# Optimization experiments

Hardware: AMD Instinct MI355X
Metric: run time of the kernel (lower is better)

Reference implementation:

```python
import jax, jax.numpy as jnp
import numpy as np

B = 8          # batch
HID = 1024     # hidden_size
NH = 8         # query heads
KVH = 1        # kv heads (GQA)
HD = 256       # head_dim
NL = 18        # layers
MLP = 4096     # intermediate size
AH = 50        # action_horizon (suffix len)
AD = 32        # action_dim
P = 1037       # prefix_len
EPS = 1e-6
ROPE_BASE = 10000.0
SCALE = HD ** -0.5
NEG = -2.3819763e38


def _rms(x):
    return x * jax.lax.rsqrt(jnp.mean(x * x, axis=-1, keepdims=True) + EPS)


def _ada_norm(x, cond, W):
    # AdaRMS: cond -> (scale, shift, gate); normed*(1+scale)+shift, gate returned for gated residual
    scale, shift, gate = jnp.split(cond @ W, 3, axis=-1)
    return _rms(x) * (1.0 + scale[:, None, :]) + shift[:, None, :], gate[:, None, :]


def _rope(x, pos):
    # x: [B, heads, S, HD], pos: [B, S]; HF rotate-half convention
    inv = 1.0 / (ROPE_BASE ** (jnp.arange(0, HD, 2, dtype=jnp.float32) / HD))
    freqs = pos[:, :, None].astype(jnp.float32) * inv          # [B,S,HD/2]
    cos = jnp.tile(jnp.cos(freqs), (1, 1, 2))[:, None]          # [B,1,S,HD]
    sin = jnp.tile(jnp.sin(freqs), (1, 1, 2))[:, None]
    x1, x2 = jnp.split(x, 2, axis=-1)
    return x * cos + jnp.concatenate([-x2, x1], axis=-1) * sin


def setup_inputs() -> dict:
    key = jax.random.key(0)
    ks = jax.random.split(key, 24)
    s = 0.02
    return {
        'prefix_keys': jax.random.normal(ks[0], (B, NL, KVH, P, HD), jnp.float32),
        'prefix_values': jax.random.normal(ks[1], (B, NL, KVH, P, HD), jnp.float32),
        'prefix_pad_masks': jnp.ones((B, P), dtype=bool),
        'x_t': jax.random.normal(ks[2], (B, AH, AD), jnp.float32),
        'timestep': jax.random.uniform(ks[3], (B,), jnp.float32),
        'Wq': jax.random.normal(ks[4], (NL, HID, NH * HD), jnp.float32) * s,
        'Wk': jax.random.normal(ks[5], (NL, HID, KVH * HD), jnp.float32) * s,
        'Wv': jax.random.normal(ks[6], (NL, HID, KVH * HD), jnp.float32) * s,
        'Wo': jax.random.normal(ks[7], (NL, NH * HD, HID), jnp.float32) * s,
        'Wg': jax.random.normal(ks[8], (NL, HID, MLP), jnp.float32) * s,
        'Wu': jax.random.normal(ks[9], (NL, HID, MLP), jnp.float32) * s,
        'Wd': jax.random.normal(ks[10], (NL, MLP, HID), jnp.float32) * s,
        'A1': jax.random.normal(ks[11], (NL, HID, 3 * HID), jnp.float32) * s,
        'A2': jax.random.normal(ks[12], (NL, HID, 3 * HID), jnp.float32) * s,
        'Af': jax.random.normal(ks[13], (HID, 3 * HID), jnp.float32) * s,
        'W_act_in': jax.random.normal(ks[14], (AD, HID), jnp.float32) * s,
        'b_act_in': jnp.zeros((HID,), jnp.float32),
        'W_act_out': jax.random.normal(ks[15], (HID, AD), jnp.float32) * s,
        'b_act_out': jnp.zeros((AD,), jnp.float32),
        'W_t_in': jax.random.normal(ks[16], (HID, HID), jnp.float32) * s,
        'b_t_in': jnp.zeros((HID,), jnp.float32),
        'W_t_out': jax.random.normal(ks[17], (HID, HID), jnp.float32) * s,
        'b_t_out': jnp.zeros((HID,), jnp.float32),
    }


def reference(prefix_keys, prefix_values, prefix_pad_masks, x_t, timestep,
              Wq, Wk, Wv, Wo, Wg, Wu, Wd, A1, A2, Af,
              W_act_in, b_act_in, W_act_out, b_act_out,
              W_t_in, b_t_in, W_t_out, b_t_out):
    b = x_t.shape[0]
    # --- time embedding (sinusoidal over log-spaced periods) -> AdaRMS cond ---
    frac = jnp.linspace(0.0, 1.0, HID // 2)
    period = 0.004 * (4.0 / 0.004) ** frac
    sin_in = (2.0 * jnp.pi / period)[None, :] * timestep[:, None]
    temb = jnp.concatenate([jnp.sin(sin_in), jnp.cos(sin_in)], axis=1)  # [B,HID]
    cond = jax.nn.silu(jax.nn.silu(temb @ W_t_in + b_t_in) @ W_t_out + b_t_out)

    # --- action input projection ---
    h = x_t @ W_act_in + b_act_in  # [B,AH,HID]

    # --- attention mask & positions ---
    # suffix att_masks = [1,0,...,0] -> cumsum constant -> suffix block fully visible
    suf_att = jnp.ones((b, AH, AH), dtype=bool)
    s2p = jnp.broadcast_to(prefix_pad_masks[:, None, :], (b, AH, P))
    full = jnp.concatenate([s2p, suf_att], axis=2)          # [B,AH,P+AH]
    bias = jnp.where(full, 0.0, NEG).astype(jnp.float32)[:, None]  # [B,1,AH,P+AH]
    offs = jnp.sum(prefix_pad_masks.astype(jnp.int32), axis=-1, keepdims=True)
    pos = offs + jnp.arange(AH)                              # [B,AH]

    def layer(hcur, p):
        wq, wk, wv, wo, wg, wu, wd, a1, a2, ck, cv = p
        normed, gate = _ada_norm(hcur, cond, a1)
        q = (normed @ wq).reshape(b, AH, NH, HD).transpose(0, 2, 1, 3)
        k = (normed @ wk).reshape(b, AH, KVH, HD).transpose(0, 2, 1, 3)
        v = (normed @ wv).reshape(b, AH, KVH, HD).transpose(0, 2, 1, 3)
        q = _rope(q, pos)
        k = _rope(k, pos)
        fk = jnp.concatenate([ck, k], axis=2)   # [B,KVH,P+AH,HD]
        fv = jnp.concatenate([cv, v], axis=2)
        rep = NH // KVH
        fk = jnp.repeat(fk, rep, axis=1)
        fv = jnp.repeat(fv, rep, axis=1)
        scores = jnp.einsum('bhqd,bhkd->bhqk', q, fk) * SCALE + bias
        attn = jax.nn.softmax(scores, axis=-1)
        o = jnp.einsum('bhqk,bhkd->bhqd', attn, fv)
        o = o.transpose(0, 2, 1, 3).reshape(b, AH, NH * HD) @ wo
        h1 = hcur + gate * o                     # gated residual 1
        n2, gate2 = _ada_norm(h1, cond, a2)
        mlp = (jax.nn.gelu(n2 @ wg, approximate=True) * (n2 @ wu)) @ wd
        return h1 + gate2 * mlp, None            # gated residual 2

    pk = jnp.moveaxis(prefix_keys, 1, 0)   # [NL,B,KVH,P,HD]
    pv = jnp.moveaxis(prefix_values, 1, 0)
    h, _ = jax.lax.scan(layer, h, (Wq, Wk, Wv, Wo, Wg, Wu, Wd, A1, A2, pk, pv))

    out, _ = _ada_norm(h, cond, Af)
    return out @ W_act_out + b_act_out  # [B,AH,AD]
```

## Files before the change

kernel.cpp:

```cpp
#include <hip/hip_runtime.h>

typedef unsigned short u16;
typedef unsigned int   u32;
typedef __attribute__((ext_vector_type(8))) short bh8;
typedef __attribute__((ext_vector_type(4))) float f4;

constexpr int BATCH = 8, HIDN = 1024, NHEAD = 8, HD = 256, NLAY = 18, DMLP = 4096;
constexpr int AHOR = 50, ADIMN = 32, PFXN = 1037, SEQN = 1087, NSTR = 17, MR = 400, MP = 512;
constexpr float EPSV = 1e-6f, NEGV = -2.3819763e38f, QSCALE = 0.0625f;
constexpr size_t ADASL = (size_t)37 * 3 * BATCH * HIDN;

static __device__ __forceinline__ u16 f2bf(float x){
  union{float f; u32 u;} v; v.f = x;
  u32 r = (v.u + 0x7FFFu + ((v.u >> 16) & 1u)) >> 16;
  return (u16)r;
}
static __device__ __forceinline__ float bf2f(u16 u){
  union{u32 u; float f;} v; v.u = ((u32)u) << 16; return v.f;
}
static __device__ __forceinline__ u32 pack2(float a, float b){
  return (u32)f2bf(a) | ((u32)f2bf(b) << 16);
}
static __device__ __forceinline__ f4 MFMA(bh8 a, bh8 b, f4 c){
  return __builtin_amdgcn_mfma_f32_16x16x32_bf16(a, b, c, 0, 0, 0);
}
static __device__ __forceinline__ float siluf_(float x){ return x / (1.f + __expf(-x)); }
static __device__ __forceinline__ float geluf_(float x){
  float y = 0.7978845608028654f * (x + 0.044715f * x * x * x);
  float e = __expf(2.f * y);
  return 0.5f * x * (2.f - 2.f / (e + 1.f));
}

__global__ void k_prep(const int* __restrict__ mask, const float* __restrict__ ts,
                       float* __restrict__ temb, int* __restrict__ offs,
                       float* __restrict__ ropec, float* __restrict__ ropes)
{
  int t = threadIdx.x;
  {
    int b = t >> 5, l = t & 31;
    const int* mp = mask + b * PFXN;
    int s = 0;
    for (int k = l; k < PFXN; k += 32) s += (mp[k] != 0);
    #pragma unroll
    for (int off = 16; off >= 1; off >>= 1) s += __shfl_xor(s, off);
    if (l == 0) offs[b] = s;
  }
  for (int i = t; i < BATCH * 512; i += 256){
    int b = i >> 9, j = i & 511;
    float frac = (float)j * (1.0f / 511.0f);
    float period = 0.004f * __expf(frac * 6.907755278982137f);
    float arg = (6.283185307179586f / period) * ts[b];
    float s, c; sincosf(arg, &s, &c);
    temb[b * HIDN + j] = s;
    temb[b * HIDN + 512 + j] = c;
  }
  __syncthreads();
  for (int i = t; i < BATCH * AHOR * 128; i += 256){
    int d = i & 127, bt = i >> 7, b = bt / AHOR, tt = bt % AHOR;
    float inv = __expf(-((float)d * (1.f / 128.f)) * 9.210340371976184f);
    float arg = (float)(offs[b] + tt) * inv;
    float s, c; sincosf(arg, &s, &c);
    ropec[i] = c; ropes[i] = s;
  }
}

__global__ void k_tproj(const float* __restrict__ X, const float* __restrict__ W,
                        const float* __restrict__ bias, float* __restrict__ out)
{
  __shared__ float xs[BATCH * HIDN];
  __shared__ float red[BATCH][8][32];
  int t = threadIdx.x;
  for (int i = t; i < BATCH * HIDN; i += 256) xs[i] = X[i];
  __syncthreads();
  int c = t & 31, kp = t >> 5;
  int c0 = blockIdx.x * 32;
  float acc[BATCH];
  #pragma unroll
  for (int b = 0; b < BATCH; ++b) acc[b] = 0.f;
  for (int k = kp * 128; k < kp * 128 + 128; ++k){
    float w = W[(size_t)k * HIDN + c0 + c];
    #pragma unroll
    for (int b = 0; b < BATCH; ++b) acc[b] += xs[b * HIDN + k] * w;
  }
  #pragma unroll
  for (int b = 0; b < BATCH; ++b) red[b][kp][c] = acc[b];
  __syncthreads();
  int b2 = t >> 5, c2 = t & 31;
  float s = bias[c0 + c2];
  #pragma unroll
  for (int kp2 = 0; kp2 < 8; ++kp2) s += red[b2][kp2][c2];
  out[b2 * HIDN + c0 + c2] = siluf_(s);
}

__global__ void k_ada_part(const float* __restrict__ cond, const float* __restrict__ A1,
                           const float* __restrict__ A2, const float* __restrict__ Af,
                           float* __restrict__ adap)
{
  __shared__ float cs[BATCH * 128];
  int t = threadIdx.x;
  int y = blockIdx.y, ks = blockIdx.z;
  int k0 = ks * 128;
  for (int i = t; i < BATCH * 128; i += 256){
    int b = i >> 7, kk = i & 127;
    cs[i] = cond[b * HIDN + k0 + kk];
  }
  __syncthreads();
  const float* A = (y < NLAY) ? (A1 + (size_t)y * HIDN * 3072)
                  : (y < 2 * NLAY) ? (A2 + (size_t)(y - NLAY) * HIDN * 3072) : Af;
  int n = (blockIdx.x * 256 + t) * 4;
  f4 acc[BATCH];
  #pragma unroll
  for (int b = 0; b < BATCH; ++b) acc[b] = (f4){0.f,0.f,0.f,0.f};
  const float* ap = A + (size_t)k0 * 3072 + n;
  for (int kk = 0; kk < 128; kk += 8){
    f4 av[8];
    #pragma unroll
    for (int j = 0; j < 8; ++j) av[j] = *(const f4*)(ap + (size_t)(kk + j) * 3072);
    #pragma unroll
    for (int j = 0; j < 8; ++j){
      #pragma unroll
      for (int b = 0; b < BATCH; ++b) acc[b] += av[j] * cs[b * 128 + kk + j];
    }
  }
  int comp = n >> 10, nn = n & 1023;
  float* o = adap + (size_t)ks * ADASL + ((size_t)y * 3 + comp) * BATCH * HIDN + nn;
  #pragma unroll
  for (int b = 0; b < BATCH; ++b) *(f4*)(o + b * HIDN) = acc[b];
}

__global__ void k_ada_red(const float* __restrict__ adap, float* __restrict__ ada)
{
  size_t i = ((size_t)blockIdx.x * 256 + threadIdx.x) * 8;
  f4 a0 = {0,0,0,0}, a1 = {0,0,0,0};
  #pragma unroll
  for (int ks = 0; ks < 8; ++ks){
    const float* p = adap + (size_t)ks * ADASL + i;
    a0 += *(const f4*)p;
    a1 += *(const f4*)(p + 4);
  }
  *(f4*)(ada + i) = a0;
  *(f4*)(ada + i + 4) = a1;
}

__global__ void k_hin(const float* __restrict__ xt, const float* __restrict__ W,
                      const float* __restrict__ bias, float* __restrict__ h)
{
  int r = blockIdx.x;
  int t = threadIdx.x; int c0 = t * 4;
  __shared__ float xs[ADIMN];
  if (t < ADIMN) xs[t] = xt[r * ADIMN + t];
  __syncthreads();
  float a0 = bias[c0], a1 = bias[c0+1], a2 = bias[c0+2], a3 = bias[c0+3];
  for (int k = 0; k < ADIMN; ++k){
    float x = xs[k];
    const float* wp = W + k * HIDN + c0;
    a0 += x * wp[0]; a1 += x * wp[1]; a2 += x * wp[2]; a3 += x * wp[3];
  }
  float* hp = h + (size_t)r * HIDN + c0;
  hp[0] = a0; hp[1] = a1; hp[2] = a2; hp[3] = a3;
}

__global__ void k_resnorm(int mode, int np,
    const float* __restrict__ base, const u16* __restrict__ parts,
    const float* __restrict__ gate, const float* __restrict__ sc,
    const float* __restrict__ sh, float* __restrict__ outres,
    u16* __restrict__ fragA)
{
  __shared__ float redl[4];
  int t = threadIdx.x;
  int c = t * 4;
  for (int i = 0; i < 4; ++i){
    int r = blockIdx.x * 4 + i;
    bool live = (r < MR);
    float4 v = {0.f,0.f,0.f,0.f};
    int b = live ? (r / AHOR) : 0;
    if (live){
      v = *(const float4*)(base + (size_t)r * HIDN + c);
      if (mode){
        float s0 = 0, s1 = 0, s2 = 0, s3 = 0;
        #pragma unroll 4
        for (int p = 0; p < np; ++p){
          ushort4 u4 = *(const ushort4*)(parts + ((size_t)p * MP + r) * HIDN + c);
          s0 += bf2f(u4.x); s1 += bf2f(u4.y); s2 += bf2f(u4.z); s3 += bf2f(u4.w);
        }
        float4 gp = *(const float4*)(gate + b * HIDN + c);
        v.x += gp.x * s0; v.y += gp.y * s1; v.z += gp.z * s2; v.w += gp.w * s3;
        *(float4*)(outres + (size_t)r * HIDN + c) = v;
      }
    }
    float ss = v.x*v.x + v.y*v.y + v.z*v.z + v.w*v.w;
    #pragma unroll
    for (int off = 1; off < 64; off <<= 1) ss += __shfl_xor(ss, off);
    if ((t & 63) == 0) redl[t >> 6] = ss;
    __syncthreads();
    float tot = redl[0] + redl[1] + redl[2] + redl[3];
    __syncthreads();
    u16* dst = fragA + ((size_t)(c >> 3)) * MP * 8 + (size_t)r * 8 + (c & 7);
    ushort4 ov;
    if (live){
      float rstd = rsqrtf(tot * (1.0f / HIDN) + EPSV);
      const float4 scp = *(const float4*)(sc + b * HIDN + c);
      const float4 shp = *(const float4*)(sh + b * HIDN + c);
      ov.x = f2bf(v.x * rstd * (1.f + scp.x) + shp.x);
      ov.y = f2bf(v.y * rstd * (1.f + scp.y) + shp.y);
      ov.z = f2bf(v.z * rstd * (1.f + scp.z) + shp.z);
      ov.w = f2bf(v.w * rstd * (1.f + scp.w) + shp.w);
    } else {
      ov.x = ov.y = ov.z = ov.w = 0;
    }
    *(ushort4*)dst = ov;
  }
}

template<int NOUTER>
static __device__ __forceinline__ void gemm_core64(
    const u16* __restrict__ fa,
    const float* __restrict__ Wa, int cb0,
    const float* __restrict__ Wb, int cb1,
    int wN, int kc0, u16* lds, f4 acc[4][4])
{
  const int tid = threadIdx.x;
  const int lane = tid & 63, wave = tid >> 6;
  const int l15 = lane & 15, g = lane >> 4;
  const int wrow = wave * 64;
  const int sn = tid & 63, skb = (tid >> 6) * 8;
  const float* wbase = (sn < 32) ? (Wa + cb0 + sn) : (Wb + cb1 + (sn - 32));
  const size_t krow0 = (size_t)kc0 * 8 + skb;
  float pre[3][8];
  bh8 ab[2][2][4];
  #pragma unroll
  for (int j = 0; j < 8; ++j) pre[0][j] = wbase[(krow0 + j) * wN];
  #pragma unroll
  for (int kk = 0; kk < 2; ++kk){
    const u16* ap = fa + ((size_t)(kc0 + kk * 4 + g) * MP + wrow + l15) * 8;
    #pragma unroll
    for (int mf = 0; mf < 4; ++mf) ab[0][kk][mf] = *(const bh8*)(ap + mf * 128);
  }
  if (NOUTER > 1){
    #pragma unroll
    for (int j = 0; j < 8; ++j) pre[1][j] = wbase[(krow0 + 64 + j) * wN];
  }
  if (NOUTER > 2){
    #pragma unroll
    for (int j = 0; j < 8; ++j) pre[2][j] = wbase[(krow0 + 128 + j) * wN];
  }
  { u32* dst = (u32*)(lds + sn * 88 + skb);
    dst[0] = pack2(pre[0][0], pre[0][1]); dst[1] = pack2(pre[0][2], pre[0][3]);
    dst[2] = pack2(pre[0][4], pre[0][5]); dst[3] = pack2(pre[0][6], pre[0][7]); }
  __syncthreads();
  #pragma unroll
  for (int ko = 0; ko < NOUTER; ++ko){
    u16* ldsr = lds + (ko & 1) * (64 * 88);
    if (ko + 1 < NOUTER){
      #pragma unroll
      for (int kk = 0; kk < 2; ++kk){
        const u16* ap = fa + ((size_t)(kc0 + (ko + 1) * 8 + kk * 4 + g) * MP + wrow + l15) * 8;
        #pragma unroll
        for (int mf = 0; mf < 4; ++mf) ab[(ko + 1) & 1][kk][mf] = *(const bh8*)(ap + mf * 128);
      }
    }
    if (ko + 3 < NOUTER){
      #pragma unroll
      for (int j = 0; j < 8; ++j) pre[ko % 3][j] = wbase[(krow0 + (size_t)(ko + 3) * 64 + j) * wN];
    }
    #pragma unroll
    for (int kk = 0; kk < 2; ++kk){
      bh8 bb[4];
      #pragma unroll
      for (int nf = 0; nf < 4; ++nf) bb[nf] = *(const bh8*)(ldsr + (nf * 16 + l15) * 88 + kk * 32 + g * 8);
      #pragma unroll
      for (int mf = 0; mf < 4; ++mf)
        #pragma unroll
        for (int nf = 0; nf < 4; ++nf)
          acc[mf][nf] = MFMA(ab[ko & 1][kk][mf], bb[nf], acc[mf][nf]);
    }
    if (ko + 1 < NOUTER){
      u16* ldsw = lds + ((ko + 1) & 1) * (64 * 88);
      u32* dst = (u32*)(ldsw + sn * 88 + skb);
      const float* p = pre[(ko + 1) % 3];
      dst[0] = pack2(p[0], p[1]); dst[1] = pack2(p[2], p[3]);
      dst[2] = pack2(p[4], p[5]); dst[3] = pack2(p[6], p[7]);
      __syncthreads();
    }
  }
}

template<int NOUTER>
static __device__ __forceinline__ void gemm_core32w(
    const u16* __restrict__ fa,
    const float* __restrict__ Wa, int cb0,
    const float* __restrict__ Wb, int cb1,
    int wN, u16* lds, f4 acc[4][2])
{
  const int tid = threadIdx.x;
  const int lane = tid & 63, wave = tid >> 6;
  const int l15 = lane & 15, g = lane >> 4;
  const int wrow = wave * 64;
  const int sc = tid & 31, kq = tid >> 5;
  const int kb = kq * 8;
  const float* wbase = (sc < 16) ? (Wa + cb0 + sc) : (Wb + cb1 + (sc - 16));
  float pre[3][8];
  #pragma unroll
  for (int j = 0; j < 8; ++j) pre[0][j] = wbase[(size_t)(kb + j) * wN];
  if (NOUTER > 1){
    #pragma unroll
    for (int j = 0; j < 8; ++j) pre[1][j] = wbase[(size_t)(128 + kb + j) * wN];
  }
  if (NOUTER > 2){
    #pragma unroll
    for (int j = 0; j < 8; ++j) pre[2][j] = wbase[(size_t)(256 + kb + j) * wN];
  }
  { u32* dst = (u32*)(lds + sc * 136 + kb);
    dst[0] = pack2(pre[0][0], pre[0][1]); dst[1] = pack2(pre[0][2], pre[0][3]);
    dst[2] = pack2(pre[0][4], pre[0][5]); dst[3] = pack2(pre[0][6], pre[0][7]); }
  __syncthreads();
  #pragma unroll
  for (int ko = 0; ko < NOUTER; ++ko){
    u16* ldsr = lds + (ko & 1) * (32 * 136);
    bh8 a01[2][4], a23[2][4];
    #pragma unroll
    for (int kk = 0; kk < 2; ++kk){
      const u16* ap = fa + ((size_t)(ko * 16 + kk * 4 + g) * MP + wrow + l15) * 8;
      #pragma unroll
      for (int mf = 0; mf < 4; ++mf) a01[kk][mf] = *(const bh8*)(ap + mf * 128);
    }
    if (ko + 3 < NOUTER){
      #pragma unroll
      for (int j = 0; j < 8; ++j) pre[ko % 3][j] = wbase[(size_t)((ko + 3) * 128 + kb + j) * wN];
    }
    #pragma unroll
    for (int kk = 2; kk < 4; ++kk){
      const u16* ap = fa + ((size_t)(ko * 16 + kk * 4 + g) * MP + wrow + l15) * 8;
      #pragma unroll
      for (int mf = 0; mf < 4; ++mf) a23[kk - 2][mf] = *(const bh8*)(ap + mf * 128);
    }
    #pragma unroll
    for (int kk = 0; kk < 2; ++kk){
      bh8 bb[2];
      #pragma unroll
      for (int nf = 0; nf < 2; ++nf) bb[nf] = *(const bh8*)(ldsr + (nf * 16 + l15) * 136 + kk * 32 + g * 8);
      #pragma unroll
      for (int mf = 0; mf < 4; ++mf){
        acc[mf][0] = MFMA(a01[kk][mf], bb[0], acc[mf][0]);
        acc[mf][1] = MFMA(a01[kk][mf], bb[1], acc[mf][1]);
      }
    }
    #pragma unroll
    for (int kk = 2; kk < 4; ++kk){
      bh8 bb[2];
      #pragma unroll
      for (int nf = 0; nf < 2; ++nf) bb[nf] = *(const bh8*)(ldsr + (nf * 16 + l15) * 136 + kk * 32 + g * 8);
      #pragma unroll
      for (int mf = 0; mf < 4; ++mf){
        acc[mf][0] = MFMA(a23[kk - 2][mf], bb[0], acc[mf][0]);
        acc[mf][1] = MFMA(a23[kk - 2][mf], bb[1], acc[mf][1]);
      }
    }
    if (ko + 1 < NOUTER){
      u16* ldsw = lds + ((ko + 1) & 1) * (32 * 136);
      u32* dst = (u32*)(ldsw + sc * 136 + kb);
      const float* p = pre[(ko + 1) % 3];
      dst[0] = pack2(p[0], p[1]); dst[1] = pack2(p[2], p[3]);
      dst[2] = pack2(p[4], p[5]); dst[3] = pack2(p[6], p[7]);
      __syncthreads();
    }
  }
}

__global__ __launch_bounds__(512) void k_qkvrope(
    const u16* __restrict__ n1, const float* __restrict__ Wq,
    const float* __restrict__ Wk, const float* __restrict__ Wv,
    const float* __restrict__ ropec, const float* __restrict__ ropes,
    u16* __restrict__ qf, u16* __restrict__ ks, u16* __restrict__ vs)
{
  __shared__ u16 lds[2 * 32 * 136];
  int bx = blockIdx.x;
  const float *Wa, *Wb; int cb0, cb1, wN, type, head = 0, fb = 0, d0 = 0;
  if (bx < 64){ type = 0; head = bx >> 3; fb = (bx & 7) * 16; Wa = Wq; Wb = Wq; wN = NHEAD * HD; cb0 = head * HD + fb; cb1 = cb0 + 128; }
  else if (bx < 72){ type = 1; fb = (bx - 64) * 16; Wa = Wk; Wb = Wk; wN = HD; cb0 = fb; cb1 = fb + 128; }
  else { type = 2; d0 = (bx - 72) * 32; Wa = Wv; Wb = Wv; wN = HD; cb0 = d0; cb1 = d0 + 16; }
  f4 acc[4][2];
  #pragma unroll
  for (int i = 0; i < 4; ++i)
    #pragma unroll
    for (int j = 0; j < 2; ++j) acc[i][j] = (f4){0.f, 0.f, 0.f, 0.f};
  gemm_core32w<8>(n1, Wa, cb0, Wb, cb1, wN, lds, acc);
  int tid = threadIdx.x, lane = tid & 63, wave = tid >> 6, l15 = lane & 15, g = lane >> 4;
  int wrow = wave * 64;
  #pragma unroll
  for (int mf = 0; mf < 4; ++mf)
    #pragma unroll
    for (int r = 0; r < 4; ++r){
      int row = wrow + mf * 16 + 4 * g + r;
      if (row >= MR) continue;
      int b = row / AHOR, tt = row - b * AHOR;
      float lo = acc[mf][0][r], hi = acc[mf][1][r];
      if (type == 2){
        size_t vb = ((size_t)(b * AHOR + tt)) * HD;
        vs[vb + d0 + l15] = f2bf(lo);
        vs[vb + d0 + 16 + l15] = f2bf(hi);
      } else {
        int dA = fb + l15;
        float cz = ropec[(size_t)(b * AHOR + tt) * 128 + dA];
        float sz = ropes[(size_t)(b * AHOR + tt) * 128 + dA];
        float oA = lo * cz - hi * sz;
        float oB = hi * cz + lo * sz;
        if (type == 0){
          oA *= QSCALE; oB *= QSCALE;
          int rowp = head * AHOR + tt;
          int dB = dA + 128;
          qf[((size_t)(b * 32 + (dA >> 3))) * MP * 8 + (size_t)rowp * 8 + (dA & 7)] = f2bf(oA);
          qf[((size_t)(b * 32 + (dB >> 3))) * MP * 8 + (size_t)rowp * 8 + (dB & 7)] = f2bf(oB);
        } else {
          size_t kb = ((size_t)(b * AHOR + tt)) * HD;
          ks[kb + dA] = f2bf(oA);
          ks[kb + dA + 128] = f2bf(oB);
        }
      }
    }
}

__global__ __launch_bounds__(512) void k_attn(
    const u16* __restrict__ qf, const u16* __restrict__ kss, const u16* __restrict__ vss,
    const float* __restrict__ pk, const float* __restrict__ pv,
    const int* __restrict__ mask, int layer,
    u16* __restrict__ opart, float* __restrict__ mrow, float* __restrict__ lrow)
{
  __shared__ u16 kv[64 * 264];
  __shared__ u16 plds[MP * 72];
  int s = blockIdx.x, b = blockIdx.y, z = blockIdx.z;
  int tid = threadIdx.x, lane = tid & 63, wave = tid >> 6, l15 = lane & 15, g = lane >> 4;
  int wrow = wave * 64;
  {
    int key = tid >> 3, dblk = (tid & 7) * 32;
    int kg = s * 64 + key;
    u32* dst = (u32*)(kv + key * 264 + dblk);
    if (kg < PFXN){
      const float4* src = (const float4*)(pk + (((size_t)b * NLAY + layer) * PFXN + kg) * HD + dblk);
      #pragma unroll
      for (int j = 0; j < 8; ++j){ float4 v = src[j]; dst[2*j] = pack2(v.x, v.y); dst[2*j+1] = pack2(v.z, v.w); }
    } else if (kg < SEQN){
      const u32* src = (const u32*)(kss + ((size_t)b * AHOR + (kg - PFXN)) * HD + dblk);
      #pragma unroll
      for (int j = 0; j < 16; ++j) dst[j] = src[j];
    } else {
      #pragma unroll
      for (int j = 0; j < 16; ++j) dst[j] = 0;
    }
  }
  float vreg[32];
  int vkey = tid >> 2, vdg = tid & 3;
  if (tid < 256){
    int kgv = s * 64 + vkey;
    int vdb = z * 128 + vdg * 32;
    if (kgv < PFXN){
      const float4* src = (const float4*)(pv + (((size_t)b * NLAY + layer) * PFXN + kgv) * HD + vdb);
      #pragma unroll
      for (int j = 0; j < 8; ++j){ float4 v = src[j]; vreg[4*j] = v.x; vreg[4*j+1] = v.y; vreg[4*j+2] = v.z; vreg[4*j+3] = v.w; }
    } else if (kgv < SEQN){
      const u32* src = (const u32*)(vss + ((size_t)b * AHOR + (kgv - PFXN)) * HD + vdb);
      #pragma unroll
      for (int j = 0; j < 16; ++j){ u32 u = src[j]; vreg[2*j] = bf2f((u16)(u & 0xFFFF)); vreg[2*j+1] = bf2f((u16)(u >> 16)); }
    } else {
      #pragma unroll
      for (int j = 0; j < 32; ++j) vreg[j] = 0.f;
    }
  }
  bool valid[4];
  #pragma unroll
  for (int nf = 0; nf < 4; ++nf){
    int kgc = s * 64 + nf * 16 + l15;
    valid[nf] = (kgc < PFXN) ? (mask[b * PFXN + kgc] != 0) : (kgc < SEQN);
  }
  __syncthreads();
  f4 acc[4][4];
  #pragma unroll
  for (int i = 0; i < 4; ++i)
    #pragma unroll
    for (int j = 0; j < 4; ++j) acc[i][j] = (f4){0.f,0.f,0.f,0.f};
  const u16* qb = qf + (size_t)b * 32 * MP * 8;
  #pragma unroll
  for (int ko = 0; ko < 4; ++ko)
    #pragma unroll
    for (int kk = 0; kk < 2; ++kk){
      int kc = ko * 8 + kk * 4 + g;
      bh8 a[4], bb[4];
      const u16* ap = qb + ((size_t)kc * MP + wrow + l15) * 8;
      #pragma unroll
      for (int mf = 0; mf < 4; ++mf) a[mf] = *(const bh8*)(ap + mf * 128);
      #pragma unroll
      for (int nf = 0; nf < 4; ++nf) bb[nf] = *(const bh8*)(kv + (nf * 16 + l15) * 264 + ko * 64 + kk * 32 + g * 8);
      #pragma unroll
      for (int mf = 0; mf < 4; ++mf)
        #pragma unroll
        for (int nf = 0; nf < 4; ++nf) acc[mf][nf] = MFMA(a[mf], bb[nf], acc[mf][nf]);
    }
  #pragma unroll
  for (int nf = 0; nf < 4; ++nf) if (!valid[nf]){
    #pragma unroll
    for (int mf = 0; mf < 4; ++mf){
      acc[mf][nf][0] = NEGV; acc[mf][nf][1] = NEGV; acc[mf][nf][2] = NEGV; acc[mf][nf][3] = NEGV;
    }
  }
  #pragma unroll
  for (int mf = 0; mf < 4; ++mf)
    #pragma unroll
    for (int r = 0; r < 4; ++r){
      float m0 = fmaxf(fmaxf(acc[mf][0][r], acc[mf][1][r]), fmaxf(acc[mf][2][r], acc[mf][3][r]));
      #pragma unroll
      for (int off = 1; off < 16; off <<= 1) m0 = fmaxf(m0, __shfl_xor(m0, off));
      int row = wrow + mf * 16 + 4 * g + r;
      float sum = 0.f;
      #pragma unroll
      for (int nf = 0; nf < 4; ++nf){
        float p = __expf(acc[mf][nf][r] - m0);
        sum += p;
        plds[row * 72 + nf * 16 + l15] = f2bf(p);
      }
      #pragma unroll
      for (int off = 1; off < 16; off <<= 1) sum += __shfl_xor(sum, off);
      if (z == 0 && l15 == 0){
        mrow[((size_t)b * NSTR + s) * MP + row] = m0;
        lrow[((size_t)b * NSTR + s) * MP + row] = sum;
      }
    }
  __syncthreads();
  if (tid < 256){
    #pragma unroll
    for (int j = 0; j < 32; ++j){
      int dloc = vdg * 32 + j;
      kv[dloc * 88 + ((dloc >> 5) & 3) * 8 + vkey] = f2bf(vreg[j]);
    }
  }
  __syncthreads();
  #pragma unroll
  for (int dcl = 0; dcl < 2; ++dcl){
    f4 oc[4][4];
    #pragma unroll
    for (int i = 0; i < 4; ++i)
      #pragma unroll
      for (int j = 0; j < 4; ++j) oc[i][j] = (f4){0.f,0.f,0.f,0.f};
    #pragma unroll
    for (int kk = 0; kk < 2; ++kk){
      bh8 a[4], bb[4];
      #pragma unroll
      for (int mf = 0; mf < 4; ++mf) a[mf] = *(const bh8*)(plds + (wrow + mf * 16 + l15) * 72 + kk * 32 + g * 8);
      #pragma unroll
      for (int nf = 0; nf < 4; ++nf){
        int dloc = dcl * 64 + nf * 16 + l15;
        bb[nf] = *(const bh8*)(kv + dloc * 88 + ((dloc >> 5) & 3) * 8 + kk * 32 + g * 8);
      }
      #pragma unroll
      for (int mf = 0; mf < 4; ++mf)
        #pragma unroll
        for (int nf = 0; nf < 4; ++nf) oc[mf][nf] = MFMA(a[mf], bb[nf], oc[mf][nf]);
    }
    #pragma unroll
    for (int mf = 0; mf < 4; ++mf)
      #pragma unroll
      for (int r = 0; r < 4; ++r){
        int row = wrow + mf * 16 + 4 * g + r;
        if (row < MR){
          #pragma unroll
          for (int nf = 0; nf < 4; ++nf){
            int d = z * 128 + dcl * 64 + nf * 16 + l15;
            opart[(((size_t)b * NSTR + s) * MR + row) * HD + d] = f2bf(oc[mf][nf][r]);
          }
        }
      }
  }
}

__global__ void k_comb(const u16* __restrict__ opart, const float* __restrict__ mrow,
                       const float* __restrict__ lrow, u16* __restrict__ ao)
{
  int b = blockIdx.y;
  int d = threadIdx.x;
  int r0 = blockIdx.x * 4;
  for (int i = 0; i < 4; ++i){
    int row = r0 + i;
    float M = -3.0e38f;
    for (int s2 = 0; s2 < NSTR; ++s2) M = fmaxf(M, mrow[((size_t)b * NSTR + s2) * MP + row]);
    float L = 0.f, o = 0.f;
    for (int s2 = 0; s2 < NSTR; ++s2){
      float w = __expf(mrow[((size_t)b * NSTR + s2) * MP + row] - M);
      L += w * lrow[((size_t)b * NSTR + s2) * MP + row];
      o += w * bf2f(opart[(((size_t)b * NSTR + s2) * MR + row) * HD + d]);
    }
    float val = o / L;
    int h = row / AHOR, tt = row - h * AHOR;
    int col = h * HD + d;
    int rg = b * AHOR + tt;
    ao[((size_t)(col >> 3)) * MP * 8 + (size_t)rg * 8 + (col & 7)] = f2bf(val);
  }
}

template<int NOUTER>
__global__ __launch_bounds__(512) void k_gemm_part(
    const u16* __restrict__ fa, const float* __restrict__ W, int wN,
    int kcPerSlice, u16* __restrict__ outp)
{
  __shared__ u16 lds[2 * 64 * 88];
  int n0 = blockIdx.x * 64;
  int ksl = blockIdx.y;
  f4 acc[4][4];
  #pragma unroll
  for (int i = 0; i < 4; ++i)
    #pragma unroll
    for (int j = 0; j < 4; ++j) acc[i][j] = (f4){0.f,0.f,0.f,0.f};
  gemm_core64<NOUTER>(fa, W, n0, W, n0 + 32, wN, ksl * kcPerSlice, lds, acc);
  int tid = threadIdx.x, lane = tid & 63, wave = tid >> 6, l15 = lane & 15, g = lane >> 4;
  int wrow = wave * 64;
  #pragma unroll
  for (int mf = 0; mf < 4; ++mf)
    #pragma unroll
    for (int r = 0; r < 4; ++r){
      int row = wrow + mf * 16 + 4 * g + r;
      #pragma unroll
      for (int nf = 0; nf < 4; ++nf)
        outp[((size_t)ksl * MP + row) * 1024 + n0 + nf * 16 + l15] = f2bf(acc[mf][nf][r]);
    }
}

__global__ __launch_bounds__(512) void k_mlpup(
    const u16* __restrict__ n2, const float* __restrict__ Wg, const float* __restrict__ Wu,
    u16* __restrict__ mlpf)
{
  __shared__ u16 lds[2 * 32 * 136];
  int n0 = blockIdx.x * 16;
  f4 acc[4][2];
  #pragma unroll
  for (int i = 0; i < 4; ++i)
    #pragma unroll
    for (int j = 0; j < 2; ++j) acc[i][j] = (f4){0.f,0.f,0.f,0.f};
  gemm_core32w<8>(n2, Wg, n0, Wu, n0, DMLP, lds, acc);
  int tid = threadIdx.x, lane = tid & 63, wave = tid >> 6, l15 = lane & 15, g = lane >> 4;
  int wrow = wave * 64;
  #pragma unroll
  for (int mf = 0; mf < 4; ++mf)
    #pragma unroll
    for (int r = 0; r < 4; ++r){
      int row = wrow + mf * 16 + 4 * g + r;
      int col = n0 + l15;
      float gg = acc[mf][0][r], uu = acc[mf][1][r];
      float act = geluf_(gg) * uu;
      mlpf[((size_t)(col >> 3)) * MP * 8 + (size_t)row * 8 + (col & 7)] = f2bf(act);
    }
}

__global__ void k_out(const u16* __restrict__ nfr, const float* __restrict__ W,
                      const float* __restrict__ bias, float* __restrict__ out)
{
  int t = threadIdx.x;
  int row = blockIdx.x * 8 + (t >> 5);
  int c = t & 31;
  float acc = bias[c];
  for (int k = 0; k < HIDN; ++k)
    acc += bf2f(nfr[((size_t)(k >> 3)) * MP * 8 + (size_t)row * 8 + (k & 7)]) * W[k * ADIMN + c];
  out[row * ADIMN + c] = acc;
}

extern "C" void kernel_launch(void* const* d_in, const int* in_sizes, int n_in,
                              void* d_out, int out_size, void* d_ws, size_t ws_size,
                              hipStream_t stream)
{
  const float* pk  = (const float*)d_in[0];
  const float* pv  = (const float*)d_in[1];
  const int*   msk = (const int*)d_in[2];
  const float* xt  = (const float*)d_in[3];
  const float* ts  = (const float*)d_in[4];
  const float* Wq  = (const float*)d_in[5];
  const float* Wk  = (const float*)d_in[6];
  const float* Wv  = (const float*)d_in[7];
  const float* Wo  = (const float*)d_in[8];
  const float* Wg  = (const float*)d_in[9];
  const float* Wu  = (const float*)d_in[10];
  const float* Wd  = (const float*)d_in[11];
  const float* A1  = (const float*)d_in[12];
  const float* A2  = (const float*)d_in[13];
  const float* Af  = (const float*)d_in[14];
  const float* Wai = (const float*)d_in[15];
  const float* bai = (const float*)d_in[16];
  const float* Wao = (const float*)d_in[17];
  const float* bao = (const float*)d_in[18];
  const float* Wti = (const float*)d_in[19];
  const float* bti = (const float*)d_in[20];
  const float* Wto = (const float*)d_in[21];
  const float* bto = (const float*)d_in[22];

  char* w = (char*)d_ws;
  size_t off = 0;
  auto alloc = [&](size_t bytes) -> char* {
    char* p = w + off; off += (bytes + 255) & ~(size_t)255; return p;
  };
  float* temb  = (float*)alloc((size_t)BATCH * HIDN * 4);
  float* ttmp  = (float*)alloc((size_t)BATCH * HIDN * 4);
  float* cond  = (float*)alloc((size_t)BATCH * HIDN * 4);
  int*   offs  = (int*)alloc(BATCH * 4);
  float* ropec = (float*)alloc((size_t)BATCH * AHOR * 128 * 4);
  float* ropes = (float*)alloc((size_t)BATCH * AHOR * 128 * 4);
  float* ada   = (float*)alloc(ADASL * 4);
  float* adap  = (float*)alloc(8 * ADASL * 4);
  float* h     = (float*)alloc((size_t)MR * HIDN * 4);
  float* h1    = (float*)alloc((size_t)MR * HIDN * 4);
  u16*   n1    = (u16*)alloc((size_t)128 * MP * 8 * 2);
  u16*   n2    = (u16*)alloc((size_t)128 * MP * 8 * 2);
  u16*   qf    = (u16*)alloc((size_t)BATCH * 32 * MP * 8 * 2);
  u16*   kss   = (u16*)alloc((size_t)BATCH * AHOR * HD * 2);
  u16*   vss   = (u16*)alloc((size_t)BATCH * AHOR * HD * 2);
  u16*   opart = (u16*)alloc((size_t)BATCH * NSTR * MR * HD * 2);
  float* mrow  = (float*)alloc((size_t)BATCH * NSTR * MP * 4);
  float* lrow  = (float*)alloc((size_t)BATCH * NSTR * MP * 4);
  u16*   ao    = (u16*)alloc((size_t)256 * MP * 8 * 2);
  u16*   opp   = (u16*)alloc((size_t)8 * MP * 1024 * 2);
  u16*   mlpf  = (u16*)alloc((size_t)512 * MP * 8 * 2);
  u16*   mdp   = (u16*)alloc((size_t)8 * MP * 1024 * 2);
  if (off > ws_size) return;

  k_prep<<<1, 256, 0, stream>>>(msk, ts, temb, offs, ropec, ropes);
  k_tproj<<<32, 256, 0, stream>>>(temb, Wti, bti, ttmp);
  k_tproj<<<32, 256, 0, stream>>>(ttmp, Wto, bto, cond);
  k_ada_part<<<dim3(3, 37, 8), 256, 0, stream>>>(cond, A1, A2, Af, adap);
  k_ada_red<<<444, 256, 0, stream>>>(adap, ada);
  k_hin<<<MR, 256, 0, stream>>>(xt, Wai, bai, h);

  auto AP = [&](int y, int comp){ return ada + ((size_t)y * 3 + comp) * BATCH * HIDN; };

  k_resnorm<<<128, 256, 0, stream>>>(0, 0, h, nullptr, nullptr, AP(0,0), AP(0,1), nullptr, n1);

  for (int l = 0; l < NLAY; ++l){
    k_qkvrope<<<80, 512, 0, stream>>>(n1, Wq + (size_t)l * HIDN * NHEAD * HD,
                                      Wk + (size_t)l * HIDN * HD, Wv + (size_t)l * HIDN * HD,
                                      ropec, ropes, qf, kss, vss);
    k_attn<<<dim3(NSTR, BATCH, 2), 512, 0, stream>>>(qf, kss, vss, pk, pv, msk, l, opart, mrow, lrow);
    k_comb<<<dim3(100, BATCH), 256, 0, stream>>>(opart, mrow, lrow, ao);
    k_gemm_part<4><<<dim3(16, 8), 512, 0, stream>>>(ao, Wo + (size_t)l * 2048 * 1024, 1024, 32, opp);
    k_resnorm<<<128, 256, 0, stream>>>(1, 8, h, opp, AP(l,2), AP(NLAY+l,0), AP(NLAY+l,1), h1, n2);
    k_mlpup<<<256, 512, 0, stream>>>(n2, Wg + (size_t)l * HIDN * DMLP, Wu + (size_t)l * HIDN * DMLP, mlpf);
    k_gemm_part<8><<<dim3(16, 8), 512, 0, stream>>>(mlpf, Wd + (size_t)l * DMLP * 1024, 1024, 64, mdp);
    const float* nsc = (l < NLAY - 1) ? AP(l + 1, 0) : AP(36, 0);
    const float* nsh = (l < NLAY - 1) ? AP(l + 1, 1) : AP(36, 1);
    k_resnorm<<<128, 256, 0, stream>>>(2, 8, h1, mdp, AP(NLAY+l,2), nsc, nsh, h, n1);
  }
  k_out<<<50, 256, 0, stream>>>(n1, Wao, bao, (float*)d_out);
}
```

Baseline: 3.147 ms.

## Vectorize weight loads, vectorize attention combine, double split-K slices

```diff
diff --git a/kernel.cpp b/kernel.cpp
--- a/kernel.cpp
+++ b/kernel.cpp
@@ -223,13 +223,14 @@
   const int lane = tid & 63, wave = tid >> 6;
   const int l15 = lane & 15, g = lane >> 4;
   const int wrow = wave * 64;
-  const int sn = tid & 63, skb = (tid >> 6) * 8;
-  const float* wbase = (sn < 32) ? (Wa + cb0 + sn) : (Wb + cb1 + (sn - 32));
-  const size_t krow0 = (size_t)kc0 * 8 + skb;
-  float pre[3][8];
+  const int c4 = (tid & 15) * 4;
+  const int r0 = (tid >> 4) * 2;
+  const float* wcol = (c4 < 32) ? (Wa + cb0 + c4) : (Wb + cb1 + (c4 - 32));
+  const size_t krow0 = (size_t)kc0 * 8 + r0;
+  f4 preA[3], preB[3];
   bh8 ab[2][2][4];
-  #pragma unroll
-  for (int j = 0; j < 8; ++j) pre[0][j] = wbase[(krow0 + j) * wN];
+  preA[0] = *(const f4*)(wcol + krow0 * wN);
+  preB[0] = *(const f4*)(wcol + (krow0 + 1) * wN);
   #pragma unroll
   for (int kk = 0; kk < 2; ++kk){
     const u16* ap = fa + ((size_t)(kc0 + kk * 4 + g) * MP + wrow + l15) * 8;
@@ -237,16 +238,16 @@
     for (int mf = 0; mf < 4; ++mf) ab[0][kk][mf] = *(const bh8*)(ap + mf * 128);
   }
   if (NOUTER > 1){
-    #pragma unroll
-    for (int j = 0; j < 8; ++j) pre[1][j] = wbase[(krow0 + 64 + j) * wN];
+    preA[1] = *(const f4*)(wcol + (krow0 + 64) * wN);
+    preB[1] = *(const f4*)(wcol + (krow0 + 65) * wN);
   }
   if (NOUTER > 2){
-    #pragma unroll
-    for (int j = 0; j < 8; ++j) pre[2][j] = wbase[(krow0 + 128 + j) * wN];
-  }
-  { u32* dst = (u32*)(lds + sn * 88 + skb);
-    dst[0] = pack2(pre[0][0], pre[0][1]); dst[1] = pack2(pre[0][2], pre[0][3]);
-    dst[2] = pack2(pre[0][4], pre[0][5]); dst[3] = pack2(pre[0][6], pre[0][7]); }
+    preA[2] = *(const f4*)(wcol + (krow0 + 128) * wN);
+    preB[2] = *(const f4*)(wcol + (krow0 + 129) * wN);
+  }
+  #pragma unroll
+  for (int i = 0; i < 4; ++i)
+    *(u32*)(lds + (c4 + i) * 88 + r0) = pack2(preA[0][i], preB[0][i]);
   __syncthreads();
   #pragma unroll
   for (int ko = 0; ko < NOUTER; ++ko){
@@ -260,8 +261,8 @@
       }
     }
     if (ko + 3 < NOUTER){
-      #pragma unroll
-      for (int j = 0; j < 8; ++j) pre[ko % 3][j] = wbase[(krow0 + (size_t)(ko + 3) * 64 + j) * wN];
+      preA[ko % 3] = *(const f4*)(wcol + (krow0 + (size_t)(ko + 3) * 64) * wN);
+      preB[ko % 3] = *(const f4*)(wcol + (krow0 + (size_t)(ko + 3) * 64 + 1) * wN);
     }
     #pragma unroll
     for (int kk = 0; kk < 2; ++kk){
@@ -276,10 +277,10 @@
     }
     if (ko + 1 < NOUTER){
       u16* ldsw = lds + ((ko + 1) & 1) * (64 * 88);
-      u32* dst = (u32*)(ldsw + sn * 88 + skb);
-      const float* p = pre[(ko + 1) % 3];
-      dst[0] = pack2(p[0], p[1]); dst[1] = pack2(p[2], p[3]);
-      dst[2] = pack2(p[4], p[5]); dst[3] = pack2(p[6], p[7]);
+      const int sl = (ko + 1) % 3;
+      #pragma unroll
+      for (int i = 0; i < 4; ++i)
+        *(u32*)(ldsw + (c4 + i) * 88 + r0) = pack2(preA[sl][i], preB[sl][i]);
       __syncthreads();
     }
   }
@@ -296,23 +297,23 @@
   const int lane = tid & 63, wave = tid >> 6;
   const int l15 = lane & 15, g = lane >> 4;
   const int wrow = wave * 64;
-  const int sc = tid & 31, kq = tid >> 5;
-  const int kb = kq * 8;
-  const float* wbase = (sc < 16) ? (Wa + cb0 + sc) : (Wb + cb1 + (sc - 16));
-  float pre[3][8];
-  #pragma unroll
-  for (int j = 0; j < 8; ++j) pre[0][j] = wbase[(size_t)(kb + j) * wN];
+  const int c4 = (tid & 7) * 4;
+  const int r0 = (tid >> 3) * 2;
+  const float* wcol = (c4 < 16) ? (Wa + cb0 + c4) : (Wb + cb1 + (c4 - 16));
+  f4 preA[3], preB[3];
+  preA[0] = *(const f4*)(wcol + (size_t)r0 * wN);
+  preB[0] = *(const f4*)(wcol + (size_t)(r0 + 1) * wN);
   if (NOUTER > 1){
-    #pragma unroll
-    for (int j = 0; j < 8; ++j) pre[1][j] = wbase[(size_t)(128 + kb + j) * wN];
+    preA[1] = *(const f4*)(wcol + (size_t)(128 + r0) * wN);
+    preB[1] = *(const f4*)(wcol + (size_t)(129 + r0) * wN);
   }
   if (NOUTER > 2){
-    #pragma unroll
-    for (int j = 0; j < 8; ++j) pre[2][j] = wbase[(size_t)(256 + kb + j) * wN];
-  }
-  { u32* dst = (u32*)(lds + sc * 136 + kb);
-    dst[0] = pack2(pre[0][0], pre[0][1]); dst[1] = pack2(pre[0][2], pre[0][3]);
-    dst[2] = pack2(pre[0][4], pre[0][5]); dst[3] = pack2(pre[0][6], pre[0][7]); }
+    preA[2] = *(const f4*)(wcol + (size_t)(256 + r0) * wN);
+    preB[2] = *(const f4*)(wcol + (size_t)(257 + r0) * wN);
+  }
+  #pragma unroll
+  for (int i = 0; i < 4; ++i)
+    *(u32*)(lds + (c4 + i) * 136 + r0) = pack2(preA[0][i], preB[0][i]);
   __syncthreads();
   #pragma unroll
   for (int ko = 0; ko < NOUTER; ++ko){
@@ -325,8 +326,8 @@
       for (int mf = 0; mf < 4; ++mf) a01[kk][mf] = *(const bh8*)(ap + mf * 128);
     }
     if (ko + 3 < NOUTER){
-      #pragma unroll
-      for (int j = 0; j < 8; ++j) pre[ko % 3][j] = wbase[(size_t)((ko + 3) * 128 + kb + j) * wN];
+      preA[ko % 3] = *(const f4*)(wcol + (size_t)((ko + 3) * 128 + r0) * wN);
+      preB[ko % 3] = *(const f4*)(wcol + (size_t)((ko + 3) * 128 + r0 + 1) * wN);
     }
     #pragma unroll
     for (int kk = 2; kk < 4; ++kk){
@@ -358,10 +359,10 @@
     }
     if (ko + 1 < NOUTER){
       u16* ldsw = lds + ((ko + 1) & 1) * (32 * 136);
-      u32* dst = (u32*)(ldsw + sc * 136 + kb);
-      const float* p = pre[(ko + 1) % 3];
-      dst[0] = pack2(p[0], p[1]); dst[1] = pack2(p[2], p[3]);
-      dst[2] = pack2(p[4], p[5]); dst[3] = pack2(p[6], p[7]);
+      const int sl = (ko + 1) % 3;
+      #pragma unroll
+      for (int i = 0; i < 4; ++i)
+        *(u32*)(ldsw + (c4 + i) * 136 + r0) = pack2(preA[sl][i], preB[sl][i]);
       __syncthreads();
     }
   }
@@ -575,24 +576,26 @@
                        const float* __restrict__ lrow, u16* __restrict__ ao)
 {
   int b = blockIdx.y;
-  int d = threadIdx.x;
-  int r0 = blockIdx.x * 4;
-  for (int i = 0; i < 4; ++i){
-    int row = r0 + i;
-    float M = -3.0e38f;
-    for (int s2 = 0; s2 < NSTR; ++s2) M = fmaxf(M, mrow[((size_t)b * NSTR + s2) * MP + row]);
-    float L = 0.f, o = 0.f;
-    for (int s2 = 0; s2 < NSTR; ++s2){
-      float w = __expf(mrow[((size_t)b * NSTR + s2) * MP + row] - M);
-      L += w * lrow[((size_t)b * NSTR + s2) * MP + row];
-      o += w * bf2f(opart[(((size_t)b * NSTR + s2) * MR + row) * HD + d]);
-    }
-    float val = o / L;
-    int h = row / AHOR, tt = row - h * AHOR;
-    int col = h * HD + d;
-    int rg = b * AHOR + tt;
-    ao[((size_t)(col >> 3)) * MP * 8 + (size_t)rg * 8 + (col & 7)] = f2bf(val);
-  }
+  int t = threadIdx.x;
+  int d4 = (t & 63) * 4;
+  int row = blockIdx.x * 4 + (t >> 6);
+  float M = -3.0e38f;
+  for (int s2 = 0; s2 < NSTR; ++s2) M = fmaxf(M, mrow[((size_t)b * NSTR + s2) * MP + row]);
+  float L = 0.f;
+  float o0 = 0.f, o1 = 0.f, o2 = 0.f, o3 = 0.f;
+  for (int s2 = 0; s2 < NSTR; ++s2){
+    float w = __expf(mrow[((size_t)b * NSTR + s2) * MP + row] - M);
+    L += w * lrow[((size_t)b * NSTR + s2) * MP + row];
+    ushort4 u4 = *(const ushort4*)(opart + (((size_t)b * NSTR + s2) * MR + row) * HD + d4);
+    o0 += w * bf2f(u4.x); o1 += w * bf2f(u4.y); o2 += w * bf2f(u4.z); o3 += w * bf2f(u4.w);
+  }
+  float rL = 1.0f / L;
+  int h = row / AHOR, tt = row - h * AHOR;
+  int col = h * HD + d4;
+  int rg = b * AHOR + tt;
+  ushort4 ov;
+  ov.x = f2bf(o0 * rL); ov.y = f2bf(o1 * rL); ov.z = f2bf(o2 * rL); ov.w = f2bf(o3 * rL);
+  *(ushort4*)(ao + ((size_t)(col >> 3)) * MP * 8 + (size_t)rg * 8 + (col & 7)) = ov;
 }
 
 template<int NOUTER>
@@ -712,9 +715,9 @@
   float* mrow  = (float*)alloc((size_t)BATCH * NSTR * MP * 4);
   float* lrow  = (float*)alloc((size_t)BATCH * NSTR * MP * 4);
   u16*   ao    = (u16*)alloc((size_t)256 * MP * 8 * 2);
-  u16*   opp   = (u16*)alloc((size_t)8 * MP * 1024 * 2);
+  u16*   opp   = (u16*)alloc((size_t)16 * MP * 1024 * 2);
   u16*   mlpf  = (u16*)alloc((size_t)512 * MP * 8 * 2);
-  u16*   mdp   = (u16*)alloc((size_t)8 * MP * 1024 * 2);
+  u16*   mdp   = (u16*)alloc((size_t)16 * MP * 1024 * 2);
   if (off > ws_size) return;
 
   k_prep<<<1, 256, 0, stream>>>(msk, ts, temb, offs, ropec, ropes);
@@ -734,13 +737,13 @@
                                       ropec, ropes, qf, kss, vss);
     k_attn<<<dim3(NSTR, BATCH, 2), 512, 0, stream>>>(qf, kss, vss, pk, pv, msk, l, opart, mrow, lrow);
     k_comb<<<dim3(100, BATCH), 256, 0, stream>>>(opart, mrow, lrow, ao);
-    k_gemm_part<4><<<dim3(16, 8), 512, 0, stream>>>(ao, Wo + (size_t)l * 2048 * 1024, 1024, 32, opp);
-    k_resnorm<<<128, 256, 0, stream>>>(1, 8, h, opp, AP(l,2), AP(NLAY+l,0), AP(NLAY+l,1), h1, n2);
+    k_gemm_part<2><<<dim3(16, 16), 512, 0, stream>>>(ao, Wo + (size_t)l * 2048 * 1024, 1024, 16, opp);
+    k_resnorm<<<128, 256, 0, stream>>>(1, 16, h, opp, AP(l,2), AP(NLAY+l,0), AP(NLAY+l,1), h1, n2);
     k_mlpup<<<256, 512, 0, stream>>>(n2, Wg + (size_t)l * HIDN * DMLP, Wu + (size_t)l * HIDN * DMLP, mlpf);
-    k_gemm_part<8><<<dim3(16, 8), 512, 0, stream>>>(mlpf, Wd + (size_t)l * DMLP * 1024, 1024, 64, mdp);
+    k_gemm_part<4><<<dim3(16, 16), 512, 0, stream>>>(mlpf, Wd + (size_t)l * DMLP * 1024, 1024, 32, mdp);
     const float* nsc = (l < NLAY - 1) ? AP(l + 1, 0) : AP(36, 0);
     const float* nsh = (l < NLAY - 1) ? AP(l + 1, 1) : AP(36, 1);
-    k_resnorm<<<128, 256, 0, stream>>>(2, 8, h1, mdp, AP(NLAY+l,2), nsc, nsh, h, n1);
+    k_resnorm<<<128, 256, 0, stream>>>(2, 16, h1, mdp, AP(NLAY+l,2), nsc, nsh, h, n1);
   }
   k_out<<<50, 256, 0, stream>>>(n1, Wao, bao, (float*)d_out);
 }
```

New measurement: 3.072 ms. 1.02x faster.
